# Performance work log

Hardware: AMD Instinct MI355X
Metric: run time of the kernel (lower is better)

The kernel has to match this reference:

```python
import jax, jax.numpy as jnp
import numpy as np

LEAKY_ALPHA = 0.2  # tf.nn.leaky_relu default

B, N, F_IN, HID = 1, 8192, 512, 256


def setup_inputs() -> dict:
    key = jax.random.key(0)
    ks = jax.random.split(key, 4)
    seq = jax.random.normal(ks[0], (B, N, F_IN), dtype=jnp.float32)
    bias_mat = jnp.zeros((B, N, N), dtype=jnp.float32)  # 0 = edge present (fully connected mask)
    W = jax.random.normal(ks[1], (F_IN, HID), dtype=jnp.float32) * (1.0 / np.sqrt(F_IN))
    a1 = jax.random.normal(ks[2], (HID, 1), dtype=jnp.float32) * (1.0 / np.sqrt(HID))
    b1 = jnp.zeros((1,), dtype=jnp.float32)
    a2 = jax.random.normal(ks[3], (HID, 1), dtype=jnp.float32) * (1.0 / np.sqrt(HID))
    b2 = jnp.zeros((1,), dtype=jnp.float32)
    bias_zero = jnp.zeros((HID,), dtype=jnp.float32)
    return {"seq": seq, "bias_mat": bias_mat, "W": W, "a1": a1, "b1": b1,
            "a2": a2, "b2": b2, "bias_zero": bias_zero}


def reference(seq, bias_mat, W, a1, b1, a2, b2, bias_zero):
    # Conv1D(kernel=1, no bias) == per-node linear projection
    seq_fts = jnp.einsum('bnf,fh->bnh', seq, W)            # [B,N,H]
    f_1 = jnp.einsum('bnh,ho->bno', seq_fts, a1) + b1      # [B,N,1]
    f_2 = jnp.einsum('bnh,ho->bno', seq_fts, a2) + b2      # [B,N,1]
    logits = f_1 + jnp.swapaxes(f_2, 1, 2)                 # [B,N,N] outer-sum
    scores = jnp.where(logits > 0, logits, LEAKY_ALPHA * logits) + bias_mat
    coefs = jax.nn.softmax(scores, axis=-1)                # masked softmax over neighbors
    vals = jnp.einsum('bnm,bmh->bnh', coefs, seq_fts)      # aggregation
    ret = vals + bias_zero
    return jax.nn.elu(ret)
```

## Files before the change

### kernel.cpp

```cpp
#include <hip/hip_runtime.h>
#include <hip/hip_bf16.h>
#include <stdint.h>

#define NN 8192
#define FIN 512
#define HID 256

typedef short bf16x8 __attribute__((ext_vector_type(8)));
typedef float f32x4 __attribute__((ext_vector_type(4)));

__device__ __forceinline__ uint32_t pk2(float lo, float hi) {
  uint32_t a = __float_as_uint(lo), b = __float_as_uint(hi);
  a = (a + 0x7FFFu + ((a >> 16) & 1u)) >> 16;
  b = (b + 0x7FFFu + ((b >> 16) & 1u)) >> 16;
  return a | (b << 16);
}

#define OFF_SEQB   0u
#define OFF_WTB    8388608u
#define OFF_FTST   8650752u
#define OFF_F1     12845056u
#define OFF_F2     12877824u
#define OFF_Z      12910592u
#define OFF_F2MAX  12943360u

__global__ void k_cvt_seq(const float* __restrict__ seq, short* __restrict__ seqb) {
  int i = (blockIdx.x * 256 + threadIdx.x) * 4;
  float4 v = *(const float4*)(seq + i);
  uint2 o; o.x = pk2(v.x, v.y); o.y = pk2(v.z, v.w);
  *(uint2*)(seqb + i) = o;
}

__global__ void k_wt(const float* __restrict__ W, short* __restrict__ WTb) {
  int h = blockIdx.x;
  int t = threadIdx.x;
  int k = t * 2;
  float w0 = W[k * 256 + h], w1 = W[(k + 1) * 256 + h];
  ((uint32_t*)(WTb + h * 512))[t] = pk2(w0, w1);
}

__global__ __launch_bounds__(256) void k_proj(
    const short* __restrict__ seqb, const short* __restrict__ WTb,
    const float* __restrict__ a1, const float* __restrict__ b1,
    const float* __restrict__ a2, const float* __restrict__ b2,
    short* __restrict__ ftsP, float* __restrict__ f1g, float* __restrict__ f2g,
    uint32_t* __restrict__ f2maxenc) {
  __shared__ short At[64][72];
  __shared__ float f1a[64], f2a[64];
  const int t = threadIdx.x;
  const int l = t & 63, w = t >> 6;
  const int lr = l & 15, lg = l >> 4;
  const int R0 = blockIdx.x * 64;
  const int srow = t >> 2, scol = (t & 3) * 16;
  f32x4 acc[4][4] = {};
  if (t < 64) { f1a[t] = 0.f; f2a[t] = 0.f; }
  for (int kt = 0; kt < FIN; kt += 64) {
    uint4 s0 = *(const uint4*)(seqb + (size_t)(R0 + srow) * FIN + kt + scol);
    uint4 s1 = *(const uint4*)(seqb + (size_t)(R0 + srow) * FIN + kt + scol + 8);
    __syncthreads();
    *(uint4*)&At[srow][scol] = s0;
    *(uint4*)&At[srow][scol + 8] = s1;
    __syncthreads();
#pragma unroll
    for (int kk = 0; kk < 2; ++kk) {
      bf16x8 af[4];
#pragma unroll
      for (int mf = 0; mf < 4; ++mf)
        af[mf] = *(const bf16x8*)&At[mf * 16 + lr][kk * 32 + lg * 8];
#pragma unroll
      for (int nf = 0; nf < 4; ++nf) {
        int h = w * 64 + nf * 16 + lr;
        bf16x8 bfr = *(const bf16x8*)(WTb + h * FIN + kt + kk * 32 + lg * 8);
#pragma unroll
        for (int mf = 0; mf < 4; ++mf)
          acc[mf][nf] = __builtin_amdgcn_mfma_f32_16x16x32_bf16(af[mf], bfr, acc[mf][nf], 0, 0, 0);
      }
    }
  }
  __syncthreads();
  float a1v[4], a2v[4];
#pragma unroll
  for (int nf = 0; nf < 4; ++nf) {
    int h = w * 64 + nf * 16 + lr;
    a1v[nf] = a1[h]; a2v[nf] = a2[h];
  }
#pragma unroll
  for (int mf = 0; mf < 4; ++mf) {
    const int jo = mf * 16 + lg * 4;
    const int slot = (jo >> 3) ^ (lr & 7);
#pragma unroll
    for (int nf = 0; nf < 4; ++nf) {
      int h = w * 64 + nf * 16 + lr;
      uint2 o; o.x = pk2(acc[mf][nf][0], acc[mf][nf][1]);
      o.y = pk2(acc[mf][nf][2], acc[mf][nf][3]);
      *(uint2*)(ftsP + (size_t)blockIdx.x * 16384 + h * 64 + slot * 8 + (jo & 7)) = o;
    }
#pragma unroll
    for (int e = 0; e < 4; ++e) {
      float p1 = 0.f, p2 = 0.f;
#pragma unroll
      for (int nf = 0; nf < 4; ++nf) { p1 += acc[mf][nf][e] * a1v[nf]; p2 += acc[mf][nf][e] * a2v[nf]; }
#pragma unroll
      for (int m = 8; m >= 1; m >>= 1) { p1 += __shfl_xor(p1, m, 16); p2 += __shfl_xor(p2, m, 16); }
      if (lr == 0) {
        atomicAdd(&f1a[mf * 16 + lg * 4 + e], p1);
        atomicAdd(&f2a[mf * 16 + lg * 4 + e], p2);
      }
    }
  }
  __syncthreads();
  if (t < 64) {
    float v1 = f1a[t] + b1[0];
    float v2 = f2a[t] + b2[0];
    f1g[R0 + t] = v1; f2g[R0 + t] = v2;
    uint32_t u = __float_as_uint(v2);
    u = (u & 0x80000000u) ? ~u : (u | 0x80000000u);
    atomicMax(f2maxenc, u);
  }
}

__global__ __launch_bounds__(256, 2) void k_flash(
    const float* __restrict__ bias, const short* __restrict__ ftsP,
    const float* __restrict__ f1g, const float* __restrict__ f2g,
    const uint32_t* __restrict__ f2maxenc,
    float* __restrict__ outacc, float* __restrict__ Zg) {
  __shared__ short Vb[2][16384];
  const int t = threadIdx.x;
  const int l = t & 63, wid = t >> 6;
  const int lr = l & 15, lg = l >> 4;
  const int rbase = blockIdx.x * 64 + wid * 16;
  const int rowA = rbase + lr;
  const int jbase = blockIdx.y * 2048;
  const int jt0 = jbase >> 6;
  const int NT = 32;

  uint32_t ue = *f2maxenc;
  float f2mx = __uint_as_float((ue & 0x80000000u) ? (ue ^ 0x80000000u) : ~ue);
  float f1v = f1g[rowA];
  float xm = f1v + f2mx;
  float mr = fmaxf(xm, 0.2f * xm);

  const float* bp = bias + (size_t)rowA * NN + jbase + lg * 8;
  const float* qp = f2g + jbase + lg * 8;

  const int s0 = lg ^ (lr & 7);
  const int s1 = s0 ^ 4;

  f32x4 acc[16] = {};
  float z = 0.f;
  float4 bb[2][2], qq[2][2];
  float4 nb[2][2], nq[2][2];

#define STAGE(TT, BUF)                                                          \
  if ((TT) < NT) {                                                              \
    const short* gs = ftsP + (size_t)(jt0 + (TT)) * 16384 + wid * 4096 + l * 8; \
    _Pragma("unroll")                                                           \
    for (int c = 0; c < 8; ++c)                                                 \
      __builtin_amdgcn_global_load_lds(                                         \
          (const __attribute__((address_space(1))) void*)(gs + c * 512),        \
          (__attribute__((address_space(3))) void*)&Vb[(BUF)][wid * 4096 + c * 512], \
          16, 0, 0);                                                            \
  }
#define LOADB(TT, B, Q)                                                         \
  if ((TT) < NT) {                                                              \
    _Pragma("unroll")                                                           \
    for (int kk = 0; kk < 2; ++kk) {                                            \
      _Pragma("unroll")                                                         \
      for (int h = 0; h < 2; ++h) {                                             \
        B[kk][h] = *(const float4*)(bp + (TT) * 64 + kk * 32 + h * 4);          \
        Q[kk][h] = *(const float4*)(qp + (TT) * 64 + kk * 32 + h * 4);          \
      }                                                                         \
    }                                                                           \
  }

  STAGE(0, 0)
  STAGE(1, 1)
  LOADB(0, bb, qq)
  __syncthreads();

  for (int tt = 0; tt < NT; ++tt) {
    LOADB(tt + 1, nb, nq)

    bf16x8 A0, A1;
    {
      float p[8];
#pragma unroll
      for (int e = 0; e < 4; ++e) {
        float s = f1v + ((const float*)&qq[0][0])[e];
        float ls = fmaxf(s, 0.2f * s);
        p[e] = __expf(ls + ((const float*)&bb[0][0])[e] - mr);
      }
#pragma unroll
      for (int e = 0; e < 4; ++e) {
        float s = f1v + ((const float*)&qq[0][1])[e];
        float ls = fmaxf(s, 0.2f * s);
        p[4 + e] = __expf(ls + ((const float*)&bb[0][1])[e] - mr);
      }
      z += ((p[0] + p[1]) + (p[2] + p[3])) + ((p[4] + p[5]) + (p[6] + p[7]));
      union { bf16x8 v; uint32_t u[4]; } A;
      A.u[0] = pk2(p[0], p[1]); A.u[1] = pk2(p[2], p[3]);
      A.u[2] = pk2(p[4], p[5]); A.u[3] = pk2(p[6], p[7]);
      A0 = A.v;
    }
    {
      float p[8];
#pragma unroll
      for (int e = 0; e < 4; ++e) {
        float s = f1v + ((const float*)&qq[1][0])[e];
        float ls = fmaxf(s, 0.2f * s);
        p[e] = __expf(ls + ((const float*)&bb[1][0])[e] - mr);
      }
#pragma unroll
      for (int e = 0; e < 4; ++e) {
        float s = f1v + ((const float*)&qq[1][1])[e];
        float ls = fmaxf(s, 0.2f * s);
        p[4 + e] = __expf(ls + ((const float*)&bb[1][1])[e] - mr);
      }
      z += ((p[0] + p[1]) + (p[2] + p[3])) + ((p[4] + p[5]) + (p[6] + p[7]));
      union { bf16x8 v; uint32_t u[4]; } A;
      A.u[0] = pk2(p[0], p[1]); A.u[1] = pk2(p[2], p[3]);
      A.u[2] = pk2(p[4], p[5]); A.u[3] = pk2(p[6], p[7]);
      A1 = A.v;
    }

    {
      const int cb = tt & 1;
      const short* vr0 = &Vb[cb][lr * 64 + s0 * 8];
      const short* vr1 = &Vb[cb][lr * 64 + s1 * 8];
#pragma unroll
      for (int nf = 0; nf < 16; ++nf) {
        bf16x8 B0 = *(const bf16x8*)(vr0 + nf * 1024);
        acc[nf] = __builtin_amdgcn_mfma_f32_16x16x32_bf16(A0, B0, acc[nf], 0, 0, 0);
      }
#pragma unroll
      for (int nf = 0; nf < 16; ++nf) {
        bf16x8 B1 = *(const bf16x8*)(vr1 + nf * 1024);
        acc[nf] = __builtin_amdgcn_mfma_f32_16x16x32_bf16(A1, B1, acc[nf], 0, 0, 0);
      }
    }

    __syncthreads();
    STAGE(tt + 2, tt & 1)

#pragma unroll
    for (int kk = 0; kk < 2; ++kk)
#pragma unroll
      for (int h = 0; h < 2; ++h) { bb[kk][h] = nb[kk][h]; qq[kk][h] = nq[kk][h]; }
  }
#undef STAGE
#undef LOADB

  z += __shfl_xor(z, 16);
  z += __shfl_xor(z, 32);
  if (lg == 0) atomicAdd(&Zg[rowA], z);

#pragma unroll
  for (int nf = 0; nf < 16; ++nf) {
    int col = nf * 16 + lr;
#pragma unroll
    for (int e = 0; e < 4; ++e)
      atomicAdd(&outacc[(size_t)(rbase + lg * 4 + e) * HID + col], acc[nf][e]);
  }
}

__global__ void k_final(float* __restrict__ outp, const float* __restrict__ Zg,
                        const float* __restrict__ bz) {
  int i4 = (blockIdx.x * 256 + threadIdx.x) * 4;
  int row = i4 >> 8;
  int col = i4 & 255;
  float4 v = *(float4*)(outp + i4);
  float zr = 1.0f / Zg[row];
  float4 b = *(const float4*)(bz + col);
  float r[4] = {v.x * zr + b.x, v.y * zr + b.y, v.z * zr + b.z, v.w * zr + b.w};
#pragma unroll
  for (int e = 0; e < 4; ++e) r[e] = r[e] > 0.f ? r[e] : (__expf(r[e]) - 1.f);
  *(float4*)(outp + i4) = make_float4(r[0], r[1], r[2], r[3]);
}

extern "C" void kernel_launch(void* const* d_in, const int* in_sizes, int n_in,
                              void* d_out, int out_size, void* d_ws, size_t ws_size,
                              hipStream_t stream) {
  const float* seq  = (const float*)d_in[0];
  const float* bias = (const float*)d_in[1];
  const float* W    = (const float*)d_in[2];
  const float* a1   = (const float*)d_in[3];
  const float* b1   = (const float*)d_in[4];
  const float* a2   = (const float*)d_in[5];
  const float* b2   = (const float*)d_in[6];
  const float* bz   = (const float*)d_in[7];
  float* out = (float*)d_out;
  char* ws = (char*)d_ws;
  short* seqb = (short*)(ws + OFF_SEQB);
  short* WTb  = (short*)(ws + OFF_WTB);
  short* ftsP = (short*)(ws + OFF_FTST);
  float* f1g  = (float*)(ws + OFF_F1);
  float* f2g  = (float*)(ws + OFF_F2);
  float* Zg   = (float*)(ws + OFF_Z);
  uint32_t* f2m = (uint32_t*)(ws + OFF_F2MAX);

  hipMemsetAsync(d_out, 0, (size_t)NN * HID * 4, stream);
  hipMemsetAsync(Zg, 0, NN * 4, stream);
  hipMemsetAsync(f2m, 0, 4, stream);

  k_cvt_seq<<<4096, 256, 0, stream>>>(seq, seqb);
  k_wt<<<256, 256, 0, stream>>>(W, WTb);
  k_proj<<<128, 256, 0, stream>>>(seqb, WTb, a1, b1, a2, b2, ftsP, f1g, f2g, f2m);
  k_flash<<<dim3(128, 4), 256, 0, stream>>>(bias, ftsP, f1g, f2g, f2m, out, Zg);
  k_final<<<2048, 256, 0, stream>>>(out, Zg, bz);
}
```

Before: 156.8 us.

## Process two 16-row tiles per wave to reuse LDS V fragments

Each wave now computes 32 query rows with two accumulator sets, so each LDS-loaded V fragment feeds two MFMAs and V traffic per row halves. The column split grows from 4 to 8 chunks to keep the grid size, and the bias prefetch is rescheduled after the exp computation in place of double-buffered registers. This raises register pressure and doubles the atomic writes to the output accumulator.

```diff
diff --git a/kernel.cpp b/kernel.cpp
--- a/kernel.cpp
+++ b/kernel.cpp
@@ -128,28 +128,31 @@
   const int t = threadIdx.x;
   const int l = t & 63, wid = t >> 6;
   const int lr = l & 15, lg = l >> 4;
-  const int rbase = blockIdx.x * 64 + wid * 16;
+  const int rbase = blockIdx.x * 128 + wid * 32;
   const int rowA = rbase + lr;
-  const int jbase = blockIdx.y * 2048;
+  const int jbase = blockIdx.y * 1024;
   const int jt0 = jbase >> 6;
-  const int NT = 32;
+  const int NT = 16;
 
   uint32_t ue = *f2maxenc;
   float f2mx = __uint_as_float((ue & 0x80000000u) ? (ue ^ 0x80000000u) : ~ue);
-  float f1v = f1g[rowA];
-  float xm = f1v + f2mx;
-  float mr = fmaxf(xm, 0.2f * xm);
-
-  const float* bp = bias + (size_t)rowA * NN + jbase + lg * 8;
+  float f1v0 = f1g[rowA];
+  float f1v1 = f1g[rowA + 16];
+  float x0 = f1v0 + f2mx, x1 = f1v1 + f2mx;
+  float mr0 = fmaxf(x0, 0.2f * x0);
+  float mr1 = fmaxf(x1, 0.2f * x1);
+
+  const float* bp0 = bias + (size_t)rowA * NN + jbase + lg * 8;
+  const float* bp1 = bp0 + (size_t)16 * NN;
   const float* qp = f2g + jbase + lg * 8;
 
   const int s0 = lg ^ (lr & 7);
   const int s1 = s0 ^ 4;
 
-  f32x4 acc[16] = {};
-  float z = 0.f;
-  float4 bb[2][2], qq[2][2];
-  float4 nb[2][2], nq[2][2];
+  f32x4 acc0[16] = {};
+  f32x4 acc1[16] = {};
+  float z0 = 0.f, z1 = 0.f;
+  float4 bb0[2][2], bb1[2][2], qq[2][2];
 
 #define STAGE(TT, BUF)                                                          \
   if ((TT) < NT) {                                                              \
@@ -161,67 +164,53 @@
           (__attribute__((address_space(3))) void*)&Vb[(BUF)][wid * 4096 + c * 512], \
           16, 0, 0);                                                            \
   }
-#define LOADB(TT, B, Q)                                                         \
+#define LOADB(TT)                                                               \
   if ((TT) < NT) {                                                              \
     _Pragma("unroll")                                                           \
     for (int kk = 0; kk < 2; ++kk) {                                            \
       _Pragma("unroll")                                                         \
       for (int h = 0; h < 2; ++h) {                                             \
-        B[kk][h] = *(const float4*)(bp + (TT) * 64 + kk * 32 + h * 4);          \
-        Q[kk][h] = *(const float4*)(qp + (TT) * 64 + kk * 32 + h * 4);          \
+        bb0[kk][h] = *(const float4*)(bp0 + (TT) * 64 + kk * 32 + h * 4);       \
+        bb1[kk][h] = *(const float4*)(bp1 + (TT) * 64 + kk * 32 + h * 4);       \
+        qq[kk][h]  = *(const float4*)(qp  + (TT) * 64 + kk * 32 + h * 4);       \
       }                                                                         \
     }                                                                           \
   }
+#define EHALF(F1V, MR, BBK, QQK, ZACC, AOUT)                                    \
+  {                                                                             \
+    float p[8];                                                                 \
+    _Pragma("unroll")                                                           \
+    for (int e = 0; e < 4; ++e) {                                               \
+      float s = (F1V) + ((const float*)&QQK[0])[e];                             \
+      float ls = fmaxf(s, 0.2f * s);                                            \
+      p[e] = __expf(ls + ((const float*)&BBK[0])[e] - (MR));                    \
+    }                                                                           \
+    _Pragma("unroll")                                                           \
+    for (int e = 0; e < 4; ++e) {                                               \
+      float s = (F1V) + ((const float*)&QQK[1])[e];                             \
+      float ls = fmaxf(s, 0.2f * s);                                            \
+      p[4 + e] = __expf(ls + ((const float*)&BBK[1])[e] - (MR));                \
+    }                                                                           \
+    ZACC += ((p[0] + p[1]) + (p[2] + p[3])) + ((p[4] + p[5]) + (p[6] + p[7]));  \
+    union { bf16x8 v; uint32_t u[4]; } A;                                       \
+    A.u[0] = pk2(p[0], p[1]); A.u[1] = pk2(p[2], p[3]);                         \
+    A.u[2] = pk2(p[4], p[5]); A.u[3] = pk2(p[6], p[7]);                         \
+    AOUT = A.v;                                                                 \
+  }
 
   STAGE(0, 0)
   STAGE(1, 1)
-  LOADB(0, bb, qq)
+  LOADB(0)
   __syncthreads();
 
   for (int tt = 0; tt < NT; ++tt) {
-    LOADB(tt + 1, nb, nq)
-
-    bf16x8 A0, A1;
-    {
-      float p[8];
-#pragma unroll
-      for (int e = 0; e < 4; ++e) {
-        float s = f1v + ((const float*)&qq[0][0])[e];
-        float ls = fmaxf(s, 0.2f * s);
-        p[e] = __expf(ls + ((const float*)&bb[0][0])[e] - mr);
-      }
-#pragma unroll
-      for (int e = 0; e < 4; ++e) {
-        float s = f1v + ((const float*)&qq[0][1])[e];
-        float ls = fmaxf(s, 0.2f * s);
-        p[4 + e] = __expf(ls + ((const float*)&bb[0][1])[e] - mr);
-      }
-      z += ((p[0] + p[1]) + (p[2] + p[3])) + ((p[4] + p[5]) + (p[6] + p[7]));
-      union { bf16x8 v; uint32_t u[4]; } A;
-      A.u[0] = pk2(p[0], p[1]); A.u[1] = pk2(p[2], p[3]);
-      A.u[2] = pk2(p[4], p[5]); A.u[3] = pk2(p[6], p[7]);
-      A0 = A.v;
-    }
-    {
-      float p[8];
-#pragma unroll
-      for (int e = 0; e < 4; ++e) {
-        float s = f1v + ((const float*)&qq[1][0])[e];
-        float ls = fmaxf(s, 0.2f * s);
-        p[e] = __expf(ls + ((const float*)&bb[1][0])[e] - mr);
-      }
-#pragma unroll
-      for (int e = 0; e < 4; ++e) {
-        float s = f1v + ((const float*)&qq[1][1])[e];
-        float ls = fmaxf(s, 0.2f * s);
-        p[4 + e] = __expf(ls + ((const float*)&bb[1][1])[e] - mr);
-      }
-      z += ((p[0] + p[1]) + (p[2] + p[3])) + ((p[4] + p[5]) + (p[6] + p[7]));
-      union { bf16x8 v; uint32_t u[4]; } A;
-      A.u[0] = pk2(p[0], p[1]); A.u[1] = pk2(p[2], p[3]);
-      A.u[2] = pk2(p[4], p[5]); A.u[3] = pk2(p[6], p[7]);
-      A1 = A.v;
-    }
+    bf16x8 A0k0, A0k1, A1k0, A1k1;
+    EHALF(f1v0, mr0, bb0[0], qq[0], z0, A0k0)
+    EHALF(f1v0, mr0, bb0[1], qq[1], z0, A0k1)
+    EHALF(f1v1, mr1, bb1[0], qq[0], z1, A1k0)
+    EHALF(f1v1, mr1, bb1[1], qq[1], z1, A1k1)
+
+    LOADB(tt + 1)
 
     {
       const int cb = tt & 1;
@@ -230,36 +219,39 @@
 #pragma unroll
       for (int nf = 0; nf < 16; ++nf) {
         bf16x8 B0 = *(const bf16x8*)(vr0 + nf * 1024);
-        acc[nf] = __builtin_amdgcn_mfma_f32_16x16x32_bf16(A0, B0, acc[nf], 0, 0, 0);
+        acc0[nf] = __builtin_amdgcn_mfma_f32_16x16x32_bf16(A0k0, B0, acc0[nf], 0, 0, 0);
+        acc1[nf] = __builtin_amdgcn_mfma_f32_16x16x32_bf16(A1k0, B0, acc1[nf], 0, 0, 0);
       }
 #pragma unroll
       for (int nf = 0; nf < 16; ++nf) {
         bf16x8 B1 = *(const bf16x8*)(vr1 + nf * 1024);
-        acc[nf] = __builtin_amdgcn_mfma_f32_16x16x32_bf16(A1, B1, acc[nf], 0, 0, 0);
+        acc0[nf] = __builtin_amdgcn_mfma_f32_16x16x32_bf16(A0k1, B1, acc0[nf], 0, 0, 0);
+        acc1[nf] = __builtin_amdgcn_mfma_f32_16x16x32_bf16(A1k1, B1, acc1[nf], 0, 0, 0);
       }
     }
 
     __syncthreads();
     STAGE(tt + 2, tt & 1)
-
-#pragma unroll
-    for (int kk = 0; kk < 2; ++kk)
-#pragma unroll
-      for (int h = 0; h < 2; ++h) { bb[kk][h] = nb[kk][h]; qq[kk][h] = nq[kk][h]; }
   }
 #undef STAGE
 #undef LOADB
-
-  z += __shfl_xor(z, 16);
-  z += __shfl_xor(z, 32);
-  if (lg == 0) atomicAdd(&Zg[rowA], z);
+#undef EHALF
+
+  z0 += __shfl_xor(z0, 16); z0 += __shfl_xor(z0, 32);
+  z1 += __shfl_xor(z1, 16); z1 += __shfl_xor(z1, 32);
+  if (lg == 0) {
+    atomicAdd(&Zg[rowA], z0);
+    atomicAdd(&Zg[rowA + 16], z1);
+  }
 
 #pragma unroll
   for (int nf = 0; nf < 16; ++nf) {
     int col = nf * 16 + lr;
 #pragma unroll
-    for (int e = 0; e < 4; ++e)
-      atomicAdd(&outacc[(size_t)(rbase + lg * 4 + e) * HID + col], acc[nf][e]);
+    for (int e = 0; e < 4; ++e) {
+      atomicAdd(&outacc[(size_t)(rbase + lg * 4 + e) * HID + col], acc0[nf][e]);
+      atomicAdd(&outacc[(size_t)(rbase + 16 + lg * 4 + e) * HID + col], acc1[nf][e]);
+    }
   }
 }
 
@@ -305,6 +297,6 @@
   k_cvt_seq<<<4096, 256, 0, stream>>>(seq, seqb);
   k_wt<<<256, 256, 0, stream>>>(W, WTb);
   k_proj<<<128, 256, 0, stream>>>(seqb, WTb, a1, b1, a2, b2, ftsP, f1g, f2g, f2m);
-  k_flash<<<dim3(128, 4), 256, 0, stream>>>(bias, ftsP, f1g, f2g, f2m, out, Zg);
+  k_flash<<<dim3(64, 8), 256, 0, stream>>>(bias, ftsP, f1g, f2g, f2m, out, Zg);
   k_final<<<2048, 256, 0, stream>>>(out, Zg, bz);
 }
```

Measured after the change: 174.1 us. 11.1% more time.
